# Optimization experiments

Measured on AMD Instinct MI355X. Metric: run time of the kernel, lower is better.

Reference implementation:

```python
import jax, jax.numpy as jnp
import numpy as np

NUM_CODE = 8192
CODE_DIM = 256


def setup_inputs() -> dict:
    key = jax.random.key(0)
    k1, k2 = jax.random.split(key)
    z_e = jax.random.normal(k1, (16, CODE_DIM, 32, 32), dtype=jnp.float32)
    span = 1.0 / NUM_CODE
    codebook = jax.random.uniform(k2, (NUM_CODE, CODE_DIM), dtype=jnp.float32,
                                  minval=-span, maxval=span)
    return {"z_e": z_e, "codebook": codebook}


def reference(z_e, codebook):
    # NCHW -> NHWC
    z = jnp.transpose(z_e, (0, 2, 3, 1))  # [B,H,W,D]
    B, H, W, D = z.shape
    flat = z.reshape(-1, D)  # [N,D]
    cb = jax.lax.stop_gradient(codebook)
    # squared L2 distances without materializing [N,K,D] diff tensor
    z2 = jnp.sum(flat * flat, axis=1, keepdims=True)          # [N,1]
    c2 = jnp.sum(cb * cb, axis=1)                              # [K]
    dist = z2 - 2.0 * (flat @ cb.T) + c2[None, :]              # [N,K]
    indices = jnp.argmin(dist, axis=1)                         # [N]
    z_q_flat = cb[indices]                                     # [N,D]
    z_q = z_q_flat.reshape(B, H, W, D)
    # straight-through estimator
    z_q = z + jax.lax.stop_gradient(z_q - z)
    idx = indices.reshape(B, H, W)
    z_q = jnp.transpose(z_q, (0, 3, 1, 2))  # NHWC -> NCHW
    return z_q, idx
```

## Files before the change

### kernel.cpp

```cpp
#include <hip/hip_runtime.h>

typedef __attribute__((ext_vector_type(4))) unsigned int u32x4;
typedef __attribute__((ext_vector_type(4))) int i32x4;

union I16 { u32x4 u; i32x4 i; };

#define SA_INV   (127.0f / 12.0f)
#define SB_INV   (127.0f * 8192.0f)
#define INV_SASB ((127.0 * 127.0 * 8192.0) / 12.0)
#define WI       4500
#define FINF     3.4e38f

__device__ __forceinline__ int q8(float x, float s) {
    int q = (int)__builtin_rintf(x * s);
    return q < -127 ? -127 : (q > 127 ? 127 : q);
}

__global__ __launch_bounds__(256)
void prep_all(const float* __restrict__ z, const float* __restrict__ cb,
              u32x4* __restrict__ ahi, float* __restrict__ zt,
              float* __restrict__ z2f, float* __restrict__ c2,
              unsigned int* __restrict__ ibt, u32x4* __restrict__ bstr) {
    __shared__ double pzbuf[32 * 9];
    __shared__ float tile[32 * 257];
    int tid = threadIdx.x;
    if (blockIdx.x < 512) {
        float* t16 = tile;
        float* pc = (float*)pzbuf;
        int ct = blockIdx.x;
        int cl = tid >> 4, dseg = tid & 15;
        const float* src = cb + (size_t)(ct * 16 + cl) * 256 + dseg * 16;
        float s = 0.f;
#pragma unroll
        for (int i = 0; i < 16; ++i) { float v = src[i]; t16[cl * 257 + dseg * 16 + i] = v; s += v * v; }
        pc[cl * 17 + dseg] = s;
        __syncthreads();
        if (tid < 16) {
            float t = 0.f;
#pragma unroll
            for (int i = 0; i < 16; ++i) t += pc[tid * 17 + i];
            int code = ct * 16 + tid;
            c2[code] = t;
            int ib = (int)__builtin_rintf(t * (float)INV_SASB);
            ibt[code] = (((unsigned int)(ib + 262144)) << 6) | (unsigned int)((code >> 4) & 31);
        }
        int l = tid & 63, j = tid >> 6;
        int code_l = l & 15, k0 = j * 64 + ((l >> 4) << 4);
        u32x4 v;
#pragma unroll
        for (int d = 0; d < 4; ++d) {
            unsigned int wv = 0;
#pragma unroll
            for (int bb = 0; bb < 4; ++bb) {
                int q = q8(t16[code_l * 257 + k0 + d * 4 + bb], SB_INV);
                wv |= ((unsigned int)(q & 255)) << (8 * bb);
            }
            v[d] = wv;
        }
        bstr[(size_t)(ct * 4 + j) * 64 + l] = v;
    } else {
        int bh = blockIdx.x - 512;
        int b = bh >> 5, h = bh & 31;
        for (int e = tid; e < 8192; e += 256) {
            int d = e >> 5, w = e & 31;
            tile[w * 257 + d] = z[((size_t)(b * 256 + d) * 32 + h) * 32 + w];
        }
        __syncthreads();
        for (int e = tid; e < 8192; e += 256) {
            int w = e >> 8, d = e & 255;
            zt[(size_t)(bh * 32 + w) * 256 + d] = tile[w * 257 + d];
        }
        {
            int w = tid >> 3, seg = tid & 7;
            double s = 0.0;
#pragma unroll
            for (int d = 0; d < 32; ++d) { double v = (double)tile[w * 257 + seg * 32 + d]; s += v * v; }
            pzbuf[w * 9 + seg] = s;
        }
        __syncthreads();
        if (tid < 32) {
            double s = 0.0;
#pragma unroll
            for (int seg = 0; seg < 8; ++seg) s += pzbuf[tid * 9 + seg];
            z2f[bh * 32 + tid] = (float)s;
        }
        for (int o = tid; o < 512; o += 256) {
            int l = o & 63, j = (o >> 6) & 3, tt = o >> 8;
            int wp = tt * 16 + (l & 15);
            int k0 = j * 64 + ((l >> 4) << 4);
            u32x4 v;
#pragma unroll
            for (int d = 0; d < 4; ++d) {
                unsigned int wv = 0;
#pragma unroll
                for (int bb = 0; bb < 4; ++bb) {
                    int q = q8(-2.0f * tile[wp * 257 + k0 + d * 4 + bb], SA_INV);
                    wv |= ((unsigned int)(q & 255)) << (8 * bb);
                }
                v[d] = wv;
            }
            ahi[(size_t)bh * 512 + o] = v;
        }
    }
}

__global__ __launch_bounds__(256)
void vq_main(const u32x4* __restrict__ ahi4, const u32x4* __restrict__ bstr,
             const unsigned int* __restrict__ ibt,
             unsigned int* __restrict__ cd, int* __restrict__ ci) {
    int tid = threadIdx.x;
    int wid = tid >> 6, lane = tid & 63;
    int stripe = blockIdx.x & 15;
    int rg = blockIdx.x >> 4;
    int colc = lane & 15;
    int rt0 = rg * 8 + wid * 2;

    I16 ah[2][4];
#pragma unroll
    for (int rt = 0; rt < 2; ++rt)
#pragma unroll
        for (int j = 0; j < 4; ++j)
            ah[rt][j].u = ahi4[((size_t)(rt0 + rt) * 4 + j) * 64 + lane];

    unsigned int m1[8], m2[8];
#pragma unroll
    for (int s = 0; s < 8; ++s) { m1[s] = 0xFFFFFFFFu; m2[s] = 0xFFFFFFFFu; }

    const u32x4* p0 = bstr + (size_t)stripe * 8192 + lane;
    const u32x4* p1 = p0 + 256;
    const unsigned int* ip = ibt + stripe * 512 + colc;
    i32x4 zc = (i32x4){0, 0, 0, 0};

    I16 bfA[4], bfB[4];
    unsigned int ibA, ibB;
#pragma unroll
    for (int j = 0; j < 4; ++j) bfA[j].u = p0[j * 64];
    ibA = ip[0];

    auto tilework = [&](const I16 (&bf)[4], unsigned int ibv) {
        i32x4 acc0, acc1;
        acc0 = __builtin_amdgcn_mfma_i32_16x16x64_i8(ah[0][0].i, bf[0].i, zc, 0, 0, 0);
        acc1 = __builtin_amdgcn_mfma_i32_16x16x64_i8(ah[1][0].i, bf[0].i, zc, 0, 0, 0);
#pragma unroll
        for (int j = 1; j < 4; ++j) {
            acc0 = __builtin_amdgcn_mfma_i32_16x16x64_i8(ah[0][j].i, bf[j].i, acc0, 0, 0, 0);
            acc1 = __builtin_amdgcn_mfma_i32_16x16x64_i8(ah[1][j].i, bf[j].i, acc1, 0, 0, 0);
        }
#pragma unroll
        for (int s = 0; s < 8; ++s) {
            unsigned int av = (unsigned int)((s < 4) ? acc0[s & 3] : acc1[s & 3]);
            unsigned int key;
            asm("v_lshl_add_u32 %0, %3, 6, %4\n\t"
                "v_med3_u32 %2, %0, %1, %2\n\t"
                "v_min_u32 %1, %1, %0"
                : "=&v"(key), "+v"(m1[s]), "+v"(m2[s])
                : "v"(av), "v"(ibv));
        }
    };

    for (int t = 0; t < 32; t += 2) {
#pragma unroll
        for (int j = 0; j < 4; ++j) bfB[j].u = p1[j * 64];
        ibB = ip[(t + 1) * 16];
        tilework(bfA, ibA);
        if (t + 2 < 32) {
            p0 += 512;
#pragma unroll
            for (int j = 0; j < 4; ++j) bfA[j].u = p0[j * 64];
            ibA = ip[(t + 2) * 16];
        }
        tilework(bfB, ibB);
        p1 += 512;
    }

#pragma unroll
    for (int s = 0; s < 8; ++s) {
        int rt = s >> 2, r = s & 3;
        int row = (rt0 + rt) * 16 + (lane >> 4) * 4 + r;
        unsigned int v0 = m1[s], v1 = m2[s];
        int c0 = stripe * 512 + (int)(v0 & 63) * 16 + colc;
        int c1 = stripe * 512 + (int)(v1 & 63) * 16 + colc;
        int obase = (row * 16 + stripe) * 3;
#pragma unroll
        for (int k = 0; k < 3; ++k) {
            unsigned int bv; int bi;
            if (v1 < v0) { bv = v1; bi = c1; } else { bv = v0; bi = c0; }
#pragma unroll
            for (int mm = 1; mm < 16; mm <<= 1) {
                unsigned int ov = __shfl_xor(bv, mm, 64);
                int oi = __shfl_xor(bi, mm, 64);
                if (ov < bv || (ov == bv && oi < bi)) { bv = ov; bi = oi; }
            }
            if (colc == k) { cd[obase + k] = bv; ci[obase + k] = bi; }
            if (bi == c0) v0 = 0xFFFFFFFFu;
            if (bi == c1) v1 = 0xFFFFFFFFu;
        }
    }
}

__global__ __launch_bounds__(256)
void refine(const float* __restrict__ zt, const float* __restrict__ z2f,
            const float* __restrict__ cb, const float* __restrict__ c2,
            const unsigned int* __restrict__ cd, const int* __restrict__ ci,
            float* __restrict__ out, int* __restrict__ idxi) {
    int wid = threadIdx.x >> 6, lane = threadIdx.x & 63;
    int n = blockIdx.x * 4 + wid;
    float zq[4];
#pragma unroll
    for (int q = 0; q < 4; ++q) zq[q] = zt[(size_t)n * 256 + q * 64 + lane];
    float z2v = z2f[n];

    unsigned int kd = 0xFFFFFFFFu; int civ = 0;
    if (lane < 48) { kd = cd[n * 48 + lane]; civ = ci[n * 48 + lane]; }
    unsigned int rm = kd;
#pragma unroll
    for (int m = 32; m >= 1; m >>= 1) {
        unsigned int o = __shfl_xor(rm, m, 64);
        rm = o < rm ? o : rm;
    }
    bool active = (lane < 48) && ((kd >> 6) <= (rm >> 6) + WI);
    unsigned long long mask = __ballot(active);
    float bestd = FINF; int besti = 0x7fffffff;
    while (mask) {
        int k = __ffsll(mask) - 1;
        mask &= mask - 1;
        int cidx = __shfl(civ, k, 64);
        const float* crow = cb + (size_t)cidx * 256;
        double dot = 0.0;
#pragma unroll
        for (int q = 0; q < 4; ++q)
            dot += (double)zq[q] * (double)crow[q * 64 + lane];
#pragma unroll
        for (int m = 32; m >= 1; m >>= 1) dot += __shfl_xor(dot, m, 64);
        float Mf = (float)dot;
        float d1 = z2v - 2.0f * Mf;
        float d2 = d1 + c2[cidx];
        if (d2 < bestd || (d2 == bestd && cidx < besti)) { bestd = d2; besti = cidx; }
    }
    if (lane == 0) {
        idxi[n] = besti;
        out[4194304 + n] = (float)besti;
    }
}

__global__ void gather_out(const float* __restrict__ cb,
                           const int* __restrict__ idxi,
                           float* __restrict__ out) {
    __shared__ float tile[32 * 260];
    __shared__ int sidx[32];
    int b = blockIdx.x >> 5, h = blockIdx.x & 31;
    int tid = threadIdx.x;
    if (tid < 32) sidx[tid] = idxi[(b * 32 + h) * 32 + tid];
    __syncthreads();
    for (int e = tid; e < 2048; e += 256) {
        int w = e >> 6, d4 = e & 63;
        float4 v = *reinterpret_cast<const float4*>(cb + (size_t)sidx[w] * 256 + d4 * 4);
        *reinterpret_cast<float4*>(&tile[w * 260 + d4 * 4]) = v;
    }
    __syncthreads();
    for (int e = tid; e < 2048; e += 256) {
        int d = e >> 3, w4 = e & 7;
        float4 v;
        v.x = tile[(w4 * 4 + 0) * 260 + d];
        v.y = tile[(w4 * 4 + 1) * 260 + d];
        v.z = tile[(w4 * 4 + 2) * 260 + d];
        v.w = tile[(w4 * 4 + 3) * 260 + d];
        *reinterpret_cast<float4*>(out + (((size_t)b * 256 + d) * 32 + h) * 32 + w4 * 4) = v;
    }
}

extern "C" void kernel_launch(void* const* d_in, const int* in_sizes, int n_in,
                              void* d_out, int out_size, void* d_ws, size_t ws_size,
                              hipStream_t stream) {
    const float* z  = (const float*)d_in[0];
    const float* cb = (const float*)d_in[1];
    float* out = (float*)d_out;
    char* w = (char*)d_ws;
    u32x4* ahi  = (u32x4*)(w);
    u32x4* bstr = (u32x4*)(w + 4194304);
    float* zt   = (float*)(w + 6291456);
    float* c2   = (float*)(w + 23068672);
    unsigned int* ibt = (unsigned int*)(w + 23101440);
    float* z2f  = (float*)(w + 23134208);
    unsigned int* cd = (unsigned int*)(w + 23199744);
    int*   ci   = (int*)(w + 26345472);
    int*   idxi = (int*)(w);

    prep_all<<<1024, 256, 0, stream>>>(z, cb, ahi, zt, z2f, c2, ibt, bstr);
    vq_main<<<2048, 256, 0, stream>>>(ahi, bstr, ibt, cd, ci);
    refine<<<4096, 256, 0, stream>>>(zt, z2f, cb, c2, cd, ci, out, idxi);
    gather_out<<<512, 256, 0, stream>>>(cb, idxi, out);
}
```

Before: 161.7 us.

## Stream codebook tiles through per-wave LDS ring via async global-to-LDS loads

Replaces the register double-buffered global loads of codebook tiles in vq_main with a three-slot per-wave LDS ring filled by global_load_lds, using explicit vmcnt waits to keep three tiles in flight. The index-base table for the stripe is also staged once into shared memory. The aim is deeper prefetch and less load latency exposed between MFMA tiles, without tying up vector registers. The cost is 48KB+ of LDS per block, which may reduce occupancy, plus reliance on hand-tuned waitcnt counts and scheduling barriers.

```diff
diff --git a/kernel.cpp b/kernel.cpp
--- a/kernel.cpp
+++ b/kernel.cpp
@@ -14,6 +14,12 @@
 __device__ __forceinline__ int q8(float x, float s) {
     int q = (int)__builtin_rintf(x * s);
     return q < -127 ? -127 : (q > 127 ? 127 : q);
+}
+
+__device__ __forceinline__ void glds16(const u32x4* g, u32x4* l) {
+    __builtin_amdgcn_global_load_lds(
+        (const __attribute__((address_space(1))) unsigned int*)g,
+        (__attribute__((address_space(3))) unsigned int*)l, 16, 0, 0);
 }
 
 __global__ __launch_bounds__(256)
@@ -108,6 +114,8 @@
 void vq_main(const u32x4* __restrict__ ahi4, const u32x4* __restrict__ bstr,
              const unsigned int* __restrict__ ibt,
              unsigned int* __restrict__ cd, int* __restrict__ ci) {
+    __shared__ u32x4 ring[4][3][256];
+    __shared__ unsigned int libt[512];
     int tid = threadIdx.x;
     int wid = tid >> 6, lane = tid & 63;
     int stripe = blockIdx.x & 15;
@@ -115,6 +123,8 @@
     int colc = lane & 15;
     int rt0 = rg * 8 + wid * 2;
 
+    for (int e = tid; e < 512; e += 256) libt[e] = ibt[stripe * 512 + e];
+
     I16 ah[2][4];
 #pragma unroll
     for (int rt = 0; rt < 2; ++rt)
@@ -122,20 +132,21 @@
         for (int j = 0; j < 4; ++j)
             ah[rt][j].u = ahi4[((size_t)(rt0 + rt) * 4 + j) * 64 + lane];
 
+    __syncthreads();
+
     unsigned int m1[8], m2[8];
 #pragma unroll
     for (int s = 0; s < 8; ++s) { m1[s] = 0xFFFFFFFFu; m2[s] = 0xFFFFFFFFu; }
 
-    const u32x4* p0 = bstr + (size_t)stripe * 8192 + lane;
-    const u32x4* p1 = p0 + 256;
-    const unsigned int* ip = ibt + stripe * 512 + colc;
+    const u32x4* gt = bstr + (size_t)stripe * 8192 + lane;
+
+#pragma unroll
+    for (int t = 0; t < 3; ++t)
+#pragma unroll
+        for (int q = 0; q < 4; ++q)
+            glds16(gt + t * 256 + q * 64, &ring[wid][t][q * 64]);
+
     i32x4 zc = (i32x4){0, 0, 0, 0};
-
-    I16 bfA[4], bfB[4];
-    unsigned int ibA, ibB;
-#pragma unroll
-    for (int j = 0; j < 4; ++j) bfA[j].u = p0[j * 64];
-    ibA = ip[0];
 
     auto tilework = [&](const I16 (&bf)[4], unsigned int ibv) {
         i32x4 acc0, acc1;
@@ -158,19 +169,24 @@
         }
     };
 
-    for (int t = 0; t < 32; t += 2) {
-#pragma unroll
-        for (int j = 0; j < 4; ++j) bfB[j].u = p1[j * 64];
-        ibB = ip[(t + 1) * 16];
-        tilework(bfA, ibA);
-        if (t + 2 < 32) {
-            p0 += 512;
-#pragma unroll
-            for (int j = 0; j < 4; ++j) bfA[j].u = p0[j * 64];
-            ibA = ip[(t + 2) * 16];
-        }
-        tilework(bfB, ibB);
-        p1 += 512;
+#pragma unroll
+    for (int t = 0; t < 32; ++t) {
+        const int slot = t % 3;
+        if (t < 30)       asm volatile("s_waitcnt vmcnt(8)" ::: "memory");
+        else if (t == 30) asm volatile("s_waitcnt vmcnt(4)" ::: "memory");
+        else              asm volatile("s_waitcnt vmcnt(0)" ::: "memory");
+        __builtin_amdgcn_sched_barrier(0);
+        I16 bf[4];
+#pragma unroll
+        for (int j = 0; j < 4; ++j) bf[j].u = ring[wid][slot][j * 64 + lane];
+        unsigned int ibv = libt[t * 16 + colc];
+        tilework(bf, ibv);
+        __builtin_amdgcn_sched_barrier(0);
+        if (t < 29) {
+#pragma unroll
+            for (int q = 0; q < 4; ++q)
+                glds16(gt + (t + 3) * 256 + q * 64, &ring[wid][slot][q * 64]);
+        }
     }
 
 #pragma unroll
```

After: 178.0 us. 10.1% more time.
